# Kernel optimization log

Hardware: AMD Instinct MI355X
Metric: run time of the kernel (lower is better)

The kernel has to match this reference:

```python
import jax, jax.numpy as jnp
import numpy as np

THRESHOLD = 0.2  # relation_threshold default
LN_EPS = 1e-5


def setup_inputs() -> dict:
    key = jax.random.key(0)
    ks = jax.random.split(key, 4)
    N1, N2, F, H, R = 256, 256, 512, 512, 4
    feats_img = jax.random.normal(ks[0], (N1, F), dtype=jnp.float32)
    feats_txt = jax.random.normal(ks[1], (N2, F), dtype=jnp.float32)
    # relation_projector params (R stacked copies of the 2-layer MLP)
    W1 = jax.random.normal(ks[2], (R, H, 2 * F), dtype=jnp.float32) / np.sqrt(2 * F)
    b1 = jnp.zeros((R, H), dtype=jnp.float32)
    gamma = jnp.ones((R, H), dtype=jnp.float32)
    beta = jnp.zeros((R, H), dtype=jnp.float32)
    w2 = jax.random.normal(ks[3], (R, H), dtype=jnp.float32) / np.sqrt(H)
    b2 = jnp.zeros((R,), dtype=jnp.float32)
    return {"feats_img": feats_img, "feats_txt": feats_txt, "W1": W1, "b1": b1,
            "gamma": gamma, "beta": beta, "w2": w2, "b2": b2}


def _relation_scores(x, W1, b1, gamma, beta, w2, b2):
    """Vectorized pairwise MLP: for each relation r, score[i,j] = MLP_r(cat(x_i, x_j)).
    Returns [N, N, R]."""
    N, F = x.shape
    R = W1.shape[0]
    Wl, Wr = W1[:, :, :F], W1[:, :, F:]  # Linear on concat = left half @ x_i + right half @ x_j
    scores = []
    for r in range(R):  # small fixed loop over relations keeps peak memory at one [N,N,H] block
        a = x @ Wl[r].T                                  # [N, H]
        b = x @ Wr[r].T                                  # [N, H]
        h = a[:, None, :] + b[None, :, :] + b1[r]        # [N, N, H]
        mu = h.mean(-1, keepdims=True)
        var = h.var(-1, keepdims=True)                   # biased var, matches torch LayerNorm
        hn = (h - mu) * jax.lax.rsqrt(var + LN_EPS) * gamma[r] + beta[r]
        s = jnp.maximum(hn, 0.0) @ w2[r] + b2[r]         # [N, N]
        scores.append(s)
    return jnp.stack(scores, axis=-1)                    # [N, N, R]


def reference(feats_img, feats_txt, W1, b1, gamma, beta, w2, b2):
    # node_features = cat over modalities (node_types is a static host-side list: omitted)
    x = jnp.concatenate([feats_img, feats_txt], axis=0)  # [N, F]
    S = _relation_scores(x, W1, b1, gamma, beta, w2, b2) # [N, N, R]
    best_rel = jnp.argmax(S, axis=-1).astype(jnp.int32)  # edge_types, dense form
    best_score = S.max(axis=-1)                          # edge_weights, dense form
    N = x.shape[0]
    diag = jnp.eye(N, dtype=bool)
    edge_mask = (~diag) & (best_score > THRESHOLD)       # dense encoding of edge_index
    return x, best_score, best_rel, edge_mask
```

## Files before the change

### kernel.cpp

```cpp
#include <hip/hip_runtime.h>
#include <math.h>


namespace {
constexpr size_t PLANE  = 512 * 512;
constexpr size_t OFF_A   = 0;
constexpr size_t OFF_B   = OFF_A + 4 * PLANE;
constexpr size_t OFF_DOT = OFF_B + 4 * PLANE;
constexpr size_t OFF_S   = OFF_DOT + 8 * PLANE;
constexpr size_t OFF_MA  = OFF_S + 8 * PLANE;
constexpr size_t OFF_QA  = OFF_MA + 2048;
constexpr size_t OFF_MB  = OFF_QA + 2048;
constexpr size_t OFF_QB  = OFF_MB + 2048;
constexpr size_t OFF_GBW = OFF_QB + 2048;
}

__global__ __launch_bounds__(256) void k0_gemm(const float* __restrict__ img,
                                               const float* __restrict__ txt,
                                               const float* __restrict__ W1,
                                               const float* __restrict__ b1,
                                               float* __restrict__ ws) {
  const int b = blockIdx.x;
  const int it = b >> 6;
  const int ct = b & 63;
  const int which = ct >> 5;
  const int r = (ct >> 3) & 3;
  const int ht = ct & 7;
  const int i0 = it << 6, h0 = ht << 6;
  const int t = threadIdx.x;
  const int tx = t & 15, ty = t >> 4;

  __shared__ float Xs[16 * 68];
  __shared__ float Wsm[16 * 68];

  float acc[16], pacc[16];
#pragma unroll
  for (int p = 0; p < 16; ++p) { acc[p] = 0.f; pacc[p] = 0.f; }

  const int srow = t >> 2;
  const int sf4 = (t & 3) << 2;
  const int xi = i0 + srow;
  const float* xrow = (xi < 256) ? (img + (size_t)xi * 512)
                                 : (txt + (size_t)(xi - 256) * 512);
  const float* wrow = W1 + (size_t)(r * 512 + h0 + srow) * 1024 + which * 512;

  for (int k0 = 0; k0 < 512; k0 += 16) {
    const float4 xv = *(const float4*)(xrow + k0 + sf4);
    const float4 wv = *(const float4*)(wrow + k0 + sf4);
    __syncthreads();
    Xs[(sf4 + 0) * 68 + srow] = xv.x;
    Xs[(sf4 + 1) * 68 + srow] = xv.y;
    Xs[(sf4 + 2) * 68 + srow] = xv.z;
    Xs[(sf4 + 3) * 68 + srow] = xv.w;
    Wsm[(sf4 + 0) * 68 + srow] = wv.x;
    Wsm[(sf4 + 1) * 68 + srow] = wv.y;
    Wsm[(sf4 + 2) * 68 + srow] = wv.z;
    Wsm[(sf4 + 3) * 68 + srow] = wv.w;
    __syncthreads();
#pragma unroll
    for (int k = 0; k < 16; ++k) {
      const float4 a4 = *(const float4*)&Xs[k * 68 + 4 * ty];
      const float4 b4 = *(const float4*)&Wsm[k * 68 + 4 * tx];
      const float av[4] = {a4.x, a4.y, a4.z, a4.w};
      const float bv[4] = {b4.x, b4.y, b4.z, b4.w};
#pragma unroll
      for (int c = 0; c < 4; ++c)
#pragma unroll
        for (int d = 0; d < 4; ++d)
          pacc[c * 4 + d] = fmaf(av[c], bv[d], pacc[c * 4 + d]);
    }
#pragma unroll
    for (int p = 0; p < 16; ++p) { acc[p] += pacc[p]; pacc[p] = 0.f; }
  }

  float4 bb = make_float4(0.f, 0.f, 0.f, 0.f);
  if (which) bb = *(const float4*)(b1 + r * 512 + h0 + 4 * tx);
  float* dst = ws + (which ? OFF_B : OFF_A) + (size_t)r * PLANE;
#pragma unroll
  for (int c = 0; c < 4; ++c) {
    float4 v;
    v.x = acc[c * 4 + 0] + bb.x;
    v.y = acc[c * 4 + 1] + bb.y;
    v.z = acc[c * 4 + 2] + bb.z;
    v.w = acc[c * 4 + 3] + bb.w;
    *(float4*)(dst + (size_t)(i0 + 4 * ty + c) * 512 + h0 + 4 * tx) = v;
  }
}

__global__ __launch_bounds__(256) void k1_stats(float* __restrict__ ws,
                                                const float* __restrict__ gamma,
                                                const float* __restrict__ beta,
                                                const float* __restrict__ w2) {
  const int t = threadIdx.x;
  const int gw = (blockIdx.x * 256 + t) >> 6;
  const int lane = t & 63;
  const int which = gw >> 11;
  const int rr = (gw >> 9) & 3;
  const int row = gw & 511;
  const float* src =
      ws + (which ? OFF_B : OFF_A) + (size_t)(rr * 512 + row) * 512 + lane * 8;
  float s = 0.f, q = 0.f;
#pragma unroll
  for (int c = 0; c < 2; ++c) {
    const float4 v = *(const float4*)(src + c * 4);
    s += v.x + v.y + v.z + v.w;
    q += v.x * v.x + v.y * v.y + v.z * v.z + v.w * v.w;
  }
#pragma unroll
  for (int off = 32; off >= 1; off >>= 1) {
    s += __shfl_down(s, off, 64);
    q += __shfl_down(q, off, 64);
  }
  if (lane == 0) {
    ws[(which ? OFF_MB : OFF_MA) + rr * 512 + row] = s * (1.f / 512.f);
    ws[(which ? OFF_QB : OFF_QA) + rr * 512 + row] = q;
  }
  if (blockIdx.x < 8) {
    const int idx = blockIdx.x * 256 + t;
    float4 g;
    g.x = gamma[idx]; g.y = beta[idx]; g.z = w2[idx]; g.w = 0.f;
    *(float4*)(ws + OFF_GBW + (size_t)idx * 4) = g;
  }
}

__global__ __launch_bounds__(256) void k2_dot(float* __restrict__ ws) {
  const int b = blockIdx.x;
  const int jt = b & 7, it = (b >> 3) & 7, r = (b >> 6) & 3, ks = b >> 8;
  const int i0 = it << 6, j0 = jt << 6;
  const int kb = ks << 8;
  const int t = threadIdx.x;
  const int tx = t & 15, ty = t >> 4;

  __shared__ float As[16 * 68];
  __shared__ float Bs[16 * 68];

  float acc[16];
#pragma unroll
  for (int p = 0; p < 16; ++p) acc[p] = 0.f;

  const int srow = t >> 2, sf4 = (t & 3) << 2;
  const float* arow = ws + OFF_A + (size_t)(r * 512 + i0 + srow) * 512 + kb;
  const float* brow = ws + OFF_B + (size_t)(r * 512 + j0 + srow) * 512 + kb;

  for (int k0 = 0; k0 < 256; k0 += 16) {
    const float4 av = *(const float4*)(arow + k0 + sf4);
    const float4 bv = *(const float4*)(brow + k0 + sf4);
    __syncthreads();
    As[(sf4 + 0) * 68 + srow] = av.x;
    As[(sf4 + 1) * 68 + srow] = av.y;
    As[(sf4 + 2) * 68 + srow] = av.z;
    As[(sf4 + 3) * 68 + srow] = av.w;
    Bs[(sf4 + 0) * 68 + srow] = bv.x;
    Bs[(sf4 + 1) * 68 + srow] = bv.y;
    Bs[(sf4 + 2) * 68 + srow] = bv.z;
    Bs[(sf4 + 3) * 68 + srow] = bv.w;
    __syncthreads();
#pragma unroll
    for (int k = 0; k < 16; ++k) {
      const float4 a4 = *(const float4*)&As[k * 68 + 4 * ty];
      const float4 b4 = *(const float4*)&Bs[k * 68 + 4 * tx];
      const float av2[4] = {a4.x, a4.y, a4.z, a4.w};
      const float bv2[4] = {b4.x, b4.y, b4.z, b4.w};
#pragma unroll
      for (int c = 0; c < 4; ++c)
#pragma unroll
        for (int d = 0; d < 4; ++d)
          acc[c * 4 + d] = fmaf(av2[c], bv2[d], acc[c * 4 + d]);
    }
  }
  float* dst = ws + OFF_DOT + (size_t)ks * (4 * PLANE) + (size_t)r * PLANE;
#pragma unroll
  for (int c = 0; c < 4; ++c) {
    float4 v;
    v.x = acc[c * 4 + 0]; v.y = acc[c * 4 + 1];
    v.z = acc[c * 4 + 2]; v.w = acc[c * 4 + 3];
    *(float4*)(dst + (size_t)(i0 + 4 * ty + c) * 512 + j0 + 4 * tx) = v;
  }
}

__global__ __launch_bounds__(512) void k3_score(float* __restrict__ ws) {
  const int b = blockIdx.x;
  const int jt = b & 7, it = (b >> 3) & 7, r = (b >> 6) & 3, ks = b >> 8;
  const int i0 = it << 6, j0 = jt << 6;
  const int t = threadIdx.x;
  const int tx = t & 31, ty = t >> 5;

  __shared__ float As2[64 * 65];
  __shared__ float Bs2[64 * 65];
  __shared__ float gsS[64 * 4];

  const float4 mav = *(const float4*)(ws + OFF_MA + r * 512 + i0 + 4 * ty);
  const float4 qav = *(const float4*)(ws + OFF_QA + r * 512 + i0 + 4 * ty);
  const float2 mbv = *(const float2*)(ws + OFF_MB + r * 512 + j0 + 2 * tx);
  const float2 qbv = *(const float2*)(ws + OFF_QB + r * 512 + j0 + 2 * tx);
  const float mavA[4] = {mav.x, mav.y, mav.z, mav.w};
  const float qavA[4] = {qav.x, qav.y, qav.z, qav.w};
  const float mbA[2] = {mbv.x, mbv.y};
  const float qbA[2] = {qbv.x, qbv.y};
  float Sv[8], Tv[8], acc[8];
#pragma unroll
  for (int c = 0; c < 4; ++c) {
    const size_t doff = (size_t)r * PLANE + (size_t)(i0 + 4 * ty + c) * 512 + j0 + 2 * tx;
    const float2 d0 = *(const float2*)(ws + OFF_DOT + doff);
    const float2 d1 = *(const float2*)(ws + OFF_DOT + 4 * PLANE + doff);
    const float dA[2] = {d0.x + d1.x, d0.y + d1.y};
#pragma unroll
    for (int d = 0; d < 2; ++d) {
      const int p = c * 2 + d;
      const float mu = mavA[c] + mbA[d];
      const float msq = (qavA[c] + qbA[d] + 2.f * dA[d]) * (1.f / 512.f);
      const float var = msq - mu * mu;
      const float sv = 1.0f / sqrtf(var + 1e-5f);
      Sv[p] = sv;
      Tv[p] = -mu * sv;
      acc[p] = 0.f;
    }
  }

  const int kbase = ks << 8;
  const int srow = t >> 4, sf4 = (t & 15) << 2;
  for (int kc = 0; kc < 4; ++kc) {
    const int kb = kbase + (kc << 6);
    float4 avs[2], bvs[2];
#pragma unroll
    for (int c2 = 0; c2 < 2; ++c2) {
      avs[c2] = *(const float4*)(ws + OFF_A +
                 (size_t)(r * 512 + i0 + srow + 32 * c2) * 512 + kb + sf4);
      bvs[c2] = *(const float4*)(ws + OFF_B +
                 (size_t)(r * 512 + j0 + srow + 32 * c2) * 512 + kb + sf4);
    }
    float4 gv = make_float4(0.f, 0.f, 0.f, 0.f);
    if (t < 64) gv = *(const float4*)(ws + OFF_GBW + (size_t)(r * 512 + kb + t) * 4);
    __syncthreads();
#pragma unroll
    for (int c2 = 0; c2 < 2; ++c2) {
      const int row = srow + 32 * c2;
      As2[row * 65 + sf4 + 0] = avs[c2].x;
      As2[row * 65 + sf4 + 1] = avs[c2].y;
      As2[row * 65 + sf4 + 2] = avs[c2].z;
      As2[row * 65 + sf4 + 3] = avs[c2].w;
      Bs2[row * 65 + sf4 + 0] = bvs[c2].x;
      Bs2[row * 65 + sf4 + 1] = bvs[c2].y;
      Bs2[row * 65 + sf4 + 2] = bvs[c2].z;
      Bs2[row * 65 + sf4 + 3] = bvs[c2].w;
    }
    if (t < 64) *(float4*)(gsS + t * 4) = gv;
    __syncthreads();

    float cacc[8];
#pragma unroll
    for (int p = 0; p < 8; ++p) cacc[p] = 0.f;

#pragma unroll 4
    for (int k = 0; k < 64; ++k) {
      const float4 g = *(const float4*)(gsS + 4 * k);
      float aA[4], bB[2];
#pragma unroll
      for (int c = 0; c < 4; ++c) aA[c] = As2[(4 * ty + c) * 65 + k];
#pragma unroll
      for (int d = 0; d < 2; ++d) bB[d] = Bs2[(2 * tx + d) * 65 + k];
#pragma unroll
      for (int c = 0; c < 4; ++c)
#pragma unroll
        for (int d = 0; d < 2; ++d) {
          const int p = c * 2 + d;
          const float u = aA[c] + bB[d];
          const float pp = fmaf(u, Sv[p], Tv[p]);
          const float hn = fmaf(pp, g.x, g.y);
          const float m = fmaxf(hn, 0.f);
          cacc[p] = fmaf(m, g.z, cacc[p]);
        }
    }
#pragma unroll
    for (int p = 0; p < 8; ++p) acc[p] += cacc[p];
  }

  float* dst = ws + OFF_S + (size_t)ks * (4 * PLANE) + (size_t)r * PLANE;
#pragma unroll
  for (int c = 0; c < 4; ++c) {
    float2 v;
    v.x = acc[c * 2 + 0];
    v.y = acc[c * 2 + 1];
    *(float2*)(dst + (size_t)(i0 + 4 * ty + c) * 512 + j0 + 2 * tx) = v;
  }
}

__global__ __launch_bounds__(256) void k4_combine(const float* __restrict__ ws,
                                                  const float* __restrict__ img,
                                                  const float* __restrict__ txt,
                                                  const float* __restrict__ b2,
                                                  float* __restrict__ out) {
  const int idx = blockIdx.x * 256 + threadIdx.x;
  const int i = idx >> 9, j = idx & 511;
  const float* s0 = ws + OFF_S;
  const float* s1 = ws + OFF_S + 4 * PLANE;
  float best = -3.4e38f;
  int rel = 0;
#pragma unroll
  for (int r = 0; r < 4; ++r) {
    const float s = s0[r * PLANE + idx] + s1[r * PLANE + idx] + b2[r];
    if (s > best) { best = s; rel = r; }
  }
  out[idx] = (i < 256) ? img[idx] : txt[idx - 131072];
  out[PLANE + idx] = best;
  out[2 * PLANE + idx] = (float)rel;
  out[3 * PLANE + idx] = (i != j && (double)best > 0.2) ? 1.0f : 0.0f;
}

extern "C" void kernel_launch(void* const* d_in, const int* in_sizes, int n_in,
                              void* d_out, int out_size, void* d_ws, size_t ws_size,
                              hipStream_t stream) {
  const float* img   = (const float*)d_in[0];
  const float* txt   = (const float*)d_in[1];
  const float* W1    = (const float*)d_in[2];
  const float* b1    = (const float*)d_in[3];
  const float* gamma = (const float*)d_in[4];
  const float* beta  = (const float*)d_in[5];
  const float* w2    = (const float*)d_in[6];
  const float* b2    = (const float*)d_in[7];
  float* ws  = (float*)d_ws;
  float* out = (float*)d_out;
  (void)in_sizes; (void)n_in; (void)out_size; (void)ws_size;

  hipLaunchKernelGGL(k0_gemm,    dim3(512),  dim3(256), 0, stream, img, txt, W1, b1, ws);
  hipLaunchKernelGGL(k1_stats,   dim3(1024), dim3(256), 0, stream, ws, gamma, beta, w2);
  hipLaunchKernelGGL(k2_dot,     dim3(512),  dim3(256), 0, stream, ws);
  hipLaunchKernelGGL(k3_score,   dim3(512),  dim3(512), 0, stream, ws);
  hipLaunchKernelGGL(k4_combine, dim3(1024), dim3(256), 0, stream, ws, img, txt, b2, out);
}
```

Baseline: 195.6 us.

## Fold mean and gamma into staged operands and transpose LDS tiles for vector reads

The score kernel now subtracts the per-row means and multiplies by gamma while staging A and B into shared memory. This removes one FMA per inner-loop element, since hn becomes fma(u, S, beta). The shared tiles are stored transposed with stride 68, so the inner loop reads a float4 and a float2 instead of six scalar loads, and the gamma/beta/w2 workspace is split to fit. The costs are transposed scalar LDS stores, which may bank-conflict, and a small change in rounding order.

```diff
diff --git a/kernel.cpp b/kernel.cpp
--- a/kernel.cpp
+++ b/kernel.cpp
@@ -12,7 +12,8 @@
 constexpr size_t OFF_QA  = OFF_MA + 2048;
 constexpr size_t OFF_MB  = OFF_QA + 2048;
 constexpr size_t OFF_QB  = OFF_MB + 2048;
-constexpr size_t OFF_GBW = OFF_QB + 2048;
+constexpr size_t OFF_G   = OFF_QB + 2048;
+constexpr size_t OFF_BW  = OFF_G + 2048;
 }
 
 __global__ __launch_bounds__(256) void k0_gemm(const float* __restrict__ img,
@@ -117,9 +118,11 @@
   }
   if (blockIdx.x < 8) {
     const int idx = blockIdx.x * 256 + t;
-    float4 g;
-    g.x = gamma[idx]; g.y = beta[idx]; g.z = w2[idx]; g.w = 0.f;
-    *(float4*)(ws + OFF_GBW + (size_t)idx * 4) = g;
+    ws[OFF_G + idx] = gamma[idx];
+    float2 bw;
+    bw.x = beta[idx];
+    bw.y = w2[idx];
+    *(float2*)(ws + OFF_BW + (size_t)idx * 2) = bw;
   }
 }
 
@@ -185,9 +188,9 @@
   const int t = threadIdx.x;
   const int tx = t & 31, ty = t >> 5;
 
-  __shared__ float As2[64 * 65];
-  __shared__ float Bs2[64 * 65];
-  __shared__ float gsS[64 * 4];
+  __shared__ float As2[64 * 68];
+  __shared__ float Bs2[64 * 68];
+  __shared__ float bwS[64 * 2];
 
   const float4 mav = *(const float4*)(ws + OFF_MA + r * 512 + i0 + 4 * ty);
   const float4 qav = *(const float4*)(ws + OFF_QA + r * 512 + i0 + 4 * ty);
@@ -197,7 +200,7 @@
   const float qavA[4] = {qav.x, qav.y, qav.z, qav.w};
   const float mbA[2] = {mbv.x, mbv.y};
   const float qbA[2] = {qbv.x, qbv.y};
-  float Sv[8], Tv[8], acc[8];
+  float Sv[8], acc[8];
 #pragma unroll
   for (int c = 0; c < 4; ++c) {
     const size_t doff = (size_t)r * PLANE + (size_t)(i0 + 4 * ty + c) * 512 + j0 + 2 * tx;
@@ -210,65 +213,66 @@
       const float mu = mavA[c] + mbA[d];
       const float msq = (qavA[c] + qbA[d] + 2.f * dA[d]) * (1.f / 512.f);
       const float var = msq - mu * mu;
-      const float sv = 1.0f / sqrtf(var + 1e-5f);
-      Sv[p] = sv;
-      Tv[p] = -mu * sv;
+      Sv[p] = 1.0f / sqrtf(var + 1e-5f);
       acc[p] = 0.f;
     }
   }
 
   const int kbase = ks << 8;
   const int srow = t >> 4, sf4 = (t & 15) << 2;
+  const int ra = i0 + srow, rb = j0 + srow;
+  const float maA2[2] = {ws[OFF_MA + r * 512 + ra], ws[OFF_MA + r * 512 + ra + 32]};
+  const float mbA2[2] = {ws[OFF_MB + r * 512 + rb], ws[OFF_MB + r * 512 + rb + 32]};
+
   for (int kc = 0; kc < 4; ++kc) {
     const int kb = kbase + (kc << 6);
+    const float4 gv = *(const float4*)(ws + OFF_G + r * 512 + kb + sf4);
     float4 avs[2], bvs[2];
 #pragma unroll
     for (int c2 = 0; c2 < 2; ++c2) {
-      avs[c2] = *(const float4*)(ws + OFF_A +
-                 (size_t)(r * 512 + i0 + srow + 32 * c2) * 512 + kb + sf4);
-      bvs[c2] = *(const float4*)(ws + OFF_B +
-                 (size_t)(r * 512 + j0 + srow + 32 * c2) * 512 + kb + sf4);
-    }
-    float4 gv = make_float4(0.f, 0.f, 0.f, 0.f);
-    if (t < 64) gv = *(const float4*)(ws + OFF_GBW + (size_t)(r * 512 + kb + t) * 4);
-    __syncthreads();
-#pragma unroll
-    for (int c2 = 0; c2 < 2; ++c2) {
-      const int row = srow + 32 * c2;
-      As2[row * 65 + sf4 + 0] = avs[c2].x;
-      As2[row * 65 + sf4 + 1] = avs[c2].y;
-      As2[row * 65 + sf4 + 2] = avs[c2].z;
-      As2[row * 65 + sf4 + 3] = avs[c2].w;
-      Bs2[row * 65 + sf4 + 0] = bvs[c2].x;
-      Bs2[row * 65 + sf4 + 1] = bvs[c2].y;
-      Bs2[row * 65 + sf4 + 2] = bvs[c2].z;
-      Bs2[row * 65 + sf4 + 3] = bvs[c2].w;
-    }
-    if (t < 64) *(float4*)(gsS + t * 4) = gv;
+      avs[c2] = *(const float4*)(ws + OFF_A + (size_t)(r * 512 + ra + 32 * c2) * 512 + kb + sf4);
+      bvs[c2] = *(const float4*)(ws + OFF_B + (size_t)(r * 512 + rb + 32 * c2) * 512 + kb + sf4);
+    }
+    float2 bwv = make_float2(0.f, 0.f);
+    if (t < 64) bwv = *(const float2*)(ws + OFF_BW + (size_t)(r * 512 + kb + t) * 2);
+    __syncthreads();
+    {
+      const float ga[4] = {gv.x, gv.y, gv.z, gv.w};
+#pragma unroll
+      for (int c2 = 0; c2 < 2; ++c2) {
+        const int row = srow + 32 * c2;
+        const float aq[4] = {avs[c2].x, avs[c2].y, avs[c2].z, avs[c2].w};
+        const float bq[4] = {bvs[c2].x, bvs[c2].y, bvs[c2].z, bvs[c2].w};
+#pragma unroll
+        for (int q = 0; q < 4; ++q) {
+          As2[(sf4 + q) * 68 + row] = (aq[q] - maA2[c2]) * ga[q];
+          Bs2[(sf4 + q) * 68 + row] = (bq[q] - mbA2[c2]) * ga[q];
+        }
+      }
+    }
+    if (t < 64) *(float2*)(bwS + 2 * t) = bwv;
     __syncthreads();
 
     float cacc[8];
 #pragma unroll
     for (int p = 0; p < 8; ++p) cacc[p] = 0.f;
 
-#pragma unroll 4
+#pragma unroll 8
     for (int k = 0; k < 64; ++k) {
-      const float4 g = *(const float4*)(gsS + 4 * k);
-      float aA[4], bB[2];
-#pragma unroll
-      for (int c = 0; c < 4; ++c) aA[c] = As2[(4 * ty + c) * 65 + k];
-#pragma unroll
-      for (int d = 0; d < 2; ++d) bB[d] = Bs2[(2 * tx + d) * 65 + k];
+      const float4 aA = *(const float4*)&As2[k * 68 + 4 * ty];
+      const float2 bB = *(const float2*)&Bs2[k * 68 + 2 * tx];
+      const float2 bw = *(const float2*)&bwS[2 * k];
+      const float aq[4] = {aA.x, aA.y, aA.z, aA.w};
+      const float bq[2] = {bB.x, bB.y};
 #pragma unroll
       for (int c = 0; c < 4; ++c)
 #pragma unroll
         for (int d = 0; d < 2; ++d) {
           const int p = c * 2 + d;
-          const float u = aA[c] + bB[d];
-          const float pp = fmaf(u, Sv[p], Tv[p]);
-          const float hn = fmaf(pp, g.x, g.y);
+          const float u = aq[c] + bq[d];
+          const float hn = fmaf(u, Sv[p], bw.x);
           const float m = fmaxf(hn, 0.f);
-          cacc[p] = fmaf(m, g.z, cacc[p]);
+          cacc[p] = fmaf(m, bw.y, cacc[p]);
         }
     }
 #pragma unroll
```

New measurement: 198.9 us. Within noise of the previous version (+1.7%).
